# Optimization experiments

Hardware: AMD Instinct MI355X
Metric: run time of the kernel (lower is better)

## Reference

```python
import jax, jax.numpy as jnp
import numpy as np

N = 100000   # nodes
E = 1600000  # edges
F_IN = 256   # input features
H = 128      # hidden
C = 40       # classes


def setup_inputs() -> dict:
    key = jax.random.key(0)
    ks = jax.random.split(key, 6)
    x = jax.random.normal(ks[0], (N, F_IN), dtype=jnp.float32)
    edge_index = jax.random.randint(ks[1], (2, E), 0, N, dtype=jnp.int32)
    edge_attr = jax.random.uniform(ks[2], (E,), dtype=jnp.float32)
    # Glorot-style init like GCNConv
    W1 = jax.random.normal(ks[3], (F_IN, H), dtype=jnp.float32) * (1.0 / np.sqrt(F_IN))
    b1 = jnp.zeros((H,), dtype=jnp.float32)
    W2 = jax.random.normal(ks[4], (H, C), dtype=jnp.float32) * (1.0 / np.sqrt(H))
    b2 = jnp.zeros((C,), dtype=jnp.float32)
    return {"x": x, "edge_index": edge_index, "edge_attr": edge_attr,
            "W1": W1, "b1": b1, "W2": W2, "b2": b2}


def _gcn_norm(edge_index, edge_weight, num_nodes):
    # PyG gcn_norm: add self-loops (weight 1), symmetric D^{-1/2} A D^{-1/2}
    row, col = edge_index[0], edge_index[1]
    loop = jnp.arange(num_nodes, dtype=row.dtype)
    row = jnp.concatenate([row, loop])
    col = jnp.concatenate([col, loop])
    ew = jnp.concatenate([edge_weight, jnp.ones((num_nodes,), edge_weight.dtype)])
    deg = jax.ops.segment_sum(ew, col, num_segments=num_nodes)
    dinv = jnp.where(deg > 0, jax.lax.rsqrt(deg), 0.0)
    norm = dinv[row] * ew * dinv[col]
    return row, col, norm


def _gcn_conv(x, row, col, norm, W, b):
    h = x @ W                              # [N, out] dense transform first
    msg = h[row] * norm[:, None]           # gather source + edge scaling
    out = jax.ops.segment_sum(msg, col, num_segments=x.shape[0])  # scatter-add
    return out + b


def reference(x, edge_index, edge_attr, W1, b1, W2, b2):
    row, col, norm = _gcn_norm(edge_index, edge_attr, x.shape[0])
    h = _gcn_conv(x, row, col, norm, W1, b1)
    h = jax.nn.relu(h)
    # dropout is identity in eval mode
    h = _gcn_conv(h, row, col, norm, W2, b2)
    return jax.nn.log_softmax(h, axis=1)
```

## Files before the change

kernel.cpp:

```cpp
#include <hip/hip_runtime.h>

#define N_NODES 100000
#define N_EDGES 1600000
#define F_INPUT 256
#define H_DIM   128
#define C_DIM   40
#define NBKT    391
#define NCHK    1563
#define NGEMM1  1563

typedef short  bf8   __attribute__((ext_vector_type(8)));
typedef float  f32x4 __attribute__((ext_vector_type(4)));
typedef float  f32x2 __attribute__((ext_vector_type(2)));
typedef unsigned short u16x8 __attribute__((ext_vector_type(8)));

static __device__ __forceinline__ unsigned short f2bf(float f) {
    union { float f; unsigned u; } v; v.f = f;
    unsigned r = v.u + 0x7FFFu + ((v.u >> 16) & 1u);
    return (unsigned short)(r >> 16);
}
static __device__ __forceinline__ f32x2 bfpair(unsigned u) {
    union { unsigned u; float f; } lo, hi;
    lo.u = u << 16; hi.u = u & 0xFFFF0000u;
    return (f32x2){lo.f, hi.f};
}

__global__ void k_pre(const float* __restrict__ W1, const float* __restrict__ W2,
                      unsigned short* Wp1, unsigned short* Wp2) {
    int idx = blockIdx.x * 256 + threadIdx.x;
    if (idx < 32768) {
        int j = idx & 7, lane = (idx >> 3) & 63, ks = (idx >> 9) & 7, nt = idx >> 12;
        int m = lane & 15, q = lane >> 4;
        Wp1[idx] = f2bf(W1[(ks * 32 + q * 8 + j) * H_DIM + nt * 16 + m]);
    }
    int idx2 = idx - 32768;
    if (idx2 >= 0 && idx2 < 6144) {
        int j = idx2 & 7, lane = (idx2 >> 3) & 63, ks = (idx2 >> 9) & 3, nt = idx2 >> 11;
        int m = lane & 15, q = lane >> 4;
        int n = nt * 16 + m;
        Wp2[idx2] = (n < C_DIM) ? f2bf(W2[(ks * 32 + q * 8 + j) * C_DIM + n]) : (unsigned short)0;
    }
}

__global__ void k_hist(const int* __restrict__ col, unsigned* __restrict__ histG) {
    __shared__ unsigned histL[NBKT];
    int chunk = blockIdx.x, tid = threadIdx.x;
    for (int i = tid; i < NBKT; i += 256) histL[i] = 0;
    __syncthreads();
    int e0 = chunk * 1024 + tid;
#pragma unroll
    for (int k = 0; k < 4; k++) {
        int e = e0 + k * 256;
        if (e < N_EDGES) atomicAdd(&histL[col[e] >> 8], 1u);
    }
    __syncthreads();
    for (int i = tid; i < NBKT; i += 256) histG[(size_t)i * NCHK + chunk] = histL[i];
}

__global__ __launch_bounds__(256, 2) void k_gemm1(
        const float* __restrict__ x, const unsigned short* __restrict__ Wp,
        unsigned short* __restrict__ h) {
    __shared__ unsigned short sWp[32768];
    __shared__ unsigned short lds_out[64 * H_DIM];
    int tid = threadIdx.x;
    int wave = tid >> 6, lane = tid & 63;
    int m = lane & 15, q = lane >> 4;
    int tile = blockIdx.x;
    int row0 = tile * 64 + wave * 16;
    int rowA = row0 + m; if (rowA >= N_NODES) rowA = N_NODES - 1;
    const float* xr = x + (long)rowA * F_INPUT + q * 8;

    float4 xv[16];
#pragma unroll
    for (int ks = 0; ks < 8; ks++) {
        xv[2 * ks]     = *(const float4*)(xr + ks * 32);
        xv[2 * ks + 1] = *(const float4*)(xr + ks * 32 + 4);
    }
#pragma unroll
    for (int it = 0; it < 16; it++) {
        int idx = (it * 256 + tid) * 8;
        *(u16x8*)(sWp + idx) = *(const u16x8*)(Wp + idx);
    }
    __syncthreads();

    f32x4 acc[8];
#pragma unroll
    for (int i = 0; i < 8; i++) acc[i] = (f32x4){0.f, 0.f, 0.f, 0.f};
#pragma unroll
    for (int ks = 0; ks < 8; ks++) {
        float4 a0 = xv[2 * ks], a1 = xv[2 * ks + 1];
        bf8 a;
        a[0] = (short)f2bf(a0.x); a[1] = (short)f2bf(a0.y);
        a[2] = (short)f2bf(a0.z); a[3] = (short)f2bf(a0.w);
        a[4] = (short)f2bf(a1.x); a[5] = (short)f2bf(a1.y);
        a[6] = (short)f2bf(a1.z); a[7] = (short)f2bf(a1.w);
#pragma unroll
        for (int nt = 0; nt < 8; nt++) {
            bf8 bb = *(const bf8*)(sWp + (((nt * 8 + ks) * 64 + lane) << 3));
            acc[nt] = __builtin_amdgcn_mfma_f32_16x16x32_bf16(a, bb, acc[nt], 0, 0, 0);
        }
    }
    int lrow = wave * 16 + q * 4;
#pragma unroll
    for (int nt = 0; nt < 8; nt++)
#pragma unroll
        for (int r = 0; r < 4; r++)
            lds_out[(lrow + r) * H_DIM + nt * 16 + m] = f2bf(acc[nt][r]);
    __syncthreads();
    int valid = N_NODES - tile * 64; if (valid > 64) valid = 64;
    unsigned short* gbase = h + (size_t)tile * 64 * H_DIM;
#pragma unroll
    for (int i = 0; i < 4; i++) {
        int idx = (i * 256 + tid) * 8;
        if (idx < valid * H_DIM)
            *(u16x8*)(gbase + idx) = *(const u16x8*)(lds_out + idx);
    }
}

__global__ void k_scanB(unsigned* histG, unsigned* bktTotal) {
    __shared__ unsigned s[256];
    int B = blockIdx.x, t = threadIdx.x;
    unsigned carry = 0;
    for (int c0 = 0; c0 < NCHK; c0 += 256) {
        int idx = c0 + t;
        unsigned v = (idx < NCHK) ? histG[(size_t)B * NCHK + idx] : 0;
        s[t] = v; __syncthreads();
        for (int off = 1; off < 256; off <<= 1) {
            unsigned u = (t >= off) ? s[t - off] : 0;
            __syncthreads();
            s[t] += u;
            __syncthreads();
        }
        if (idx < NCHK) histG[(size_t)B * NCHK + idx] = s[t] - v + carry;
        unsigned tot = s[255];
        __syncthreads();
        carry += tot;
    }
    if (t == 0) bktTotal[B] = carry;
}

__global__ void k_scat1(const int* __restrict__ row, const int* __restrict__ col,
                        const float* __restrict__ ea,
                        const unsigned* __restrict__ histG,
                        const unsigned* __restrict__ bktTotal,
                        unsigned* __restrict__ bucketBase,
                        int2* __restrict__ recs) {
    __shared__ unsigned base_l[NBKT];
    __shared__ unsigned cursor[NBKT];
    __shared__ unsigned s[256];
    int blk = blockIdx.x, t = threadIdx.x;
    unsigned carry = 0;
    for (int c0 = 0; c0 < NBKT; c0 += 256) {
        int idx = c0 + t;
        unsigned v = (idx < NBKT) ? bktTotal[idx] : 0;
        s[t] = v; __syncthreads();
        for (int off = 1; off < 256; off <<= 1) {
            unsigned u = (t >= off) ? s[t - off] : 0;
            __syncthreads();
            s[t] += u;
            __syncthreads();
        }
        if (idx < NBKT) base_l[idx] = s[t] - v + carry;
        unsigned tot = s[255];
        __syncthreads();
        carry += tot;
    }
    __syncthreads();
    if (blk == 0) {
        for (int i = t; i < NBKT; i += 256) bucketBase[i] = base_l[i];
        if (t == 0) bucketBase[NBKT] = carry;
    }
    for (int i = t; i < NBKT; i += 256) {
        base_l[i] += histG[(size_t)i * NCHK + blk];
        cursor[i] = 0;
    }
    __syncthreads();
    int e0 = blk * 1024 + t;
#pragma unroll
    for (int k = 0; k < 4; k++) {
        int e = e0 + k * 256;
        if (e < N_EDGES) {
            int c = col[e];
            int bkt = c >> 8;
            unsigned r = atomicAdd(&cursor[bkt], 1u);
            int pos = (int)(base_l[bkt] + r);
            recs[pos] = make_int2((row[e] << 8) | (c & 255), __float_as_int(ea[e]));
        }
    }
}

__global__ void k_pass2a(const int2* __restrict__ recs,
                         const unsigned* __restrict__ bucketBase,
                         int* __restrict__ start, int* __restrict__ cnt,
                         float* __restrict__ dinv) {
    __shared__ unsigned cntL[256];
    __shared__ unsigned wsL[256];
    __shared__ unsigned s[256];
    int B = blockIdx.x, t = threadIdx.x;
    cntL[t] = 0; wsL[t] = 0;
    __syncthreads();
    int lo = (int)bucketBase[B], hi = (int)bucketBase[B + 1];
    for (int i = lo + t; i < hi; i += 256) {
        int2 rc = recs[i];
        int cl = rc.x & 255;
        atomicAdd(&cntL[cl], 1u);
        unsigned q = __float2uint_rn(__int_as_float(rc.y) * 65536.0f);
        atomicAdd(&wsL[cl], q);
    }
    __syncthreads();
    unsigned v = cntL[t];
    s[t] = v; __syncthreads();
    for (int off = 1; off < 256; off <<= 1) {
        unsigned u = (t >= off) ? s[t - off] : 0;
        __syncthreads();
        s[t] += u;
        __syncthreads();
    }
    int node = B * 256 + t;
    if (node < N_NODES) {
        start[node] = (int)(bucketBase[B] + s[t] - v);
        cnt[node] = (int)v;
        dinv[node] = rsqrtf((float)(65536u + wsL[t]) * (1.0f / 65536.0f));
    }
}

__global__ void k_pass2b(const int2* __restrict__ recs,
                         const unsigned* __restrict__ bucketBase,
                         const int* __restrict__ start,
                         const float* __restrict__ dinv,
                         int2* __restrict__ csr) {
    __shared__ int startL[256];
    __shared__ unsigned cur[256];
    int B = blockIdx.x, t = threadIdx.x;
    int node = B * 256 + t;
    startL[t] = (node < N_NODES) ? start[node] : 0;
    cur[t] = 0;
    __syncthreads();
    int lo = (int)bucketBase[B], hi = (int)bucketBase[B + 1];
    for (int i = lo + t; i < hi; i += 256) {
        int2 rc = recs[i];
        int cl = rc.x & 255;
        int rw = rc.x >> 8;
        float w = __int_as_float(rc.y) * dinv[rw];
        unsigned r = atomicAdd(&cur[cl], 1u);
        csr[startL[cl] + (int)r] = make_int2(rw, __float_as_int(w));
    }
}

__global__ __launch_bounds__(256) void k_agg1(
        const unsigned* __restrict__ hw, const int2* __restrict__ csr,
        const int* __restrict__ start, const int* __restrict__ cnt,
        const float* __restrict__ dinv, const float* __restrict__ b1,
        unsigned* __restrict__ h1w) {
    int c = blockIdx.x * 4 + (threadIdx.x >> 6);
    int lane = threadIdx.x & 63;
    if (c >= N_NODES) return;
    float di = dinv[c];
    int su = __builtin_amdgcn_readfirstlane(start[c]);
    int n  = __builtin_amdgcn_readfirstlane(cnt[c]);
    f32x2 acc;
    {
        f32x2 sp = bfpair(hw[(size_t)c * 64 + lane]);
        acc = (f32x2){di, di} * sp;
    }
    int i = 0;
    for (; i + 4 <= n; i += 4) {
        int2 p0 = csr[su + i], p1 = csr[su + i + 1];
        int2 p2 = csr[su + i + 2], p3 = csr[su + i + 3];
        int r0 = __builtin_amdgcn_readfirstlane(p0.x);
        int r1 = __builtin_amdgcn_readfirstlane(p1.x);
        int r2 = __builtin_amdgcn_readfirstlane(p2.x);
        int r3 = __builtin_amdgcn_readfirstlane(p3.x);
        float w0 = __int_as_float(__builtin_amdgcn_readfirstlane(p0.y));
        float w1 = __int_as_float(__builtin_amdgcn_readfirstlane(p1.y));
        float w2 = __int_as_float(__builtin_amdgcn_readfirstlane(p2.y));
        float w3 = __int_as_float(__builtin_amdgcn_readfirstlane(p3.y));
        unsigned a0 = hw[(size_t)r0 * 64 + lane];
        unsigned a1 = hw[(size_t)r1 * 64 + lane];
        unsigned a2 = hw[(size_t)r2 * 64 + lane];
        unsigned a3 = hw[(size_t)r3 * 64 + lane];
        acc += (f32x2){w0, w0} * bfpair(a0);
        acc += (f32x2){w1, w1} * bfpair(a1);
        acc += (f32x2){w2, w2} * bfpair(a2);
        acc += (f32x2){w3, w3} * bfpair(a3);
    }
    for (; i < n; i++) {
        int2 p = csr[su + i];
        int r = __builtin_amdgcn_readfirstlane(p.x);
        float w = __int_as_float(__builtin_amdgcn_readfirstlane(p.y));
        unsigned a = hw[(size_t)r * 64 + lane];
        acc += (f32x2){w, w} * bfpair(a);
    }
    float2 bb = ((const float2*)b1)[lane];
    float o0 = fmaxf(di * acc.x + bb.x, 0.f);
    float o1 = fmaxf(di * acc.y + bb.y, 0.f);
    h1w[(size_t)c * 64 + lane] = (unsigned)f2bf(o0) | ((unsigned)f2bf(o1) << 16);
}

__global__ __launch_bounds__(256, 4) void k_gemm2(const unsigned short* __restrict__ h1,
                        const unsigned short* __restrict__ Wp,
                        unsigned short* __restrict__ h2) {
    __shared__ unsigned short lds_out[64 * C_DIM];
    int tid = threadIdx.x;
    int wave = tid >> 6, lane = tid & 63;
    int m = lane & 15, q = lane >> 4;
    int row0 = blockIdx.x * 64 + wave * 16;
    int rowA = row0 + m; if (rowA >= N_NODES) rowA = N_NODES - 1;

    f32x4 acc[3];
#pragma unroll
    for (int i = 0; i < 3; i++) acc[i] = (f32x4){0.f, 0.f, 0.f, 0.f};
    const unsigned short* hr = h1 + (long)rowA * H_DIM + q * 8;
#pragma unroll
    for (int ks = 0; ks < 4; ks++) {
        bf8 a = *(const bf8*)(hr + ks * 32);
#pragma unroll
        for (int nt = 0; nt < 3; nt++) {
            bf8 b = *(const bf8*)(Wp + (((nt * 4 + ks) * 64 + lane) << 3));
            acc[nt] = __builtin_amdgcn_mfma_f32_16x16x32_bf16(a, b, acc[nt], 0, 0, 0);
        }
    }
    int lrow = wave * 16 + q * 4;
#pragma unroll
    for (int nt = 0; nt < 3; nt++)
#pragma unroll
        for (int r = 0; r < 4; r++) {
            int colo = nt * 16 + m;
            if (colo < C_DIM)
                lds_out[(lrow + r) * C_DIM + colo] = f2bf(acc[nt][r]);
        }
    __syncthreads();
    int valid = N_NODES - blockIdx.x * 64; if (valid > 64) valid = 64;
    unsigned short* gbase = h2 + (size_t)blockIdx.x * 64 * C_DIM;
    int total = valid * C_DIM;
#pragma unroll
    for (int i = 0; i < 3; i++) {
        int idx = (i * 256 + tid) * 4;
        if (idx < total)
            *(uint2*)(gbase + idx) = *(const uint2*)(lds_out + idx);
    }
}

__global__ void k_agg2(const unsigned short* __restrict__ h2, const int2* __restrict__ csr,
                       const int* __restrict__ start, const int* __restrict__ cnt,
                       const float* __restrict__ dinv, const float* __restrict__ b2,
                       float* __restrict__ out) {
    int c = (blockIdx.x * blockDim.x + threadIdx.x) >> 6;
    int lane = threadIdx.x & 63;
    if (c >= N_NODES) return;
    int eg = lane >> 3, cl = lane & 7;
    float di = dinv[c];
    int s = start[c];
    int n = cnt[c];

    float w[3]; int r[3];
#pragma unroll
    for (int t = 0; t < 3; t++) {
        int i = eg + 8 * t;
        int2 p = csr[s + ((i < n) ? i : 0)];
        bool val = (i < n);
        r[t] = val ? p.x : c;
        w[t] = val ? __int_as_float(p.y) : 0.f;
    }
    uint4 gv[3] = {{0,0,0,0},{0,0,0,0},{0,0,0,0}};
    uint4 selfv = {0, 0, 0, 0};
    if (cl < 5) {
#pragma unroll
        for (int t = 0; t < 3; t++)
            gv[t] = *(const uint4*)(h2 + (long)r[t] * C_DIM + cl * 8);
        if (eg == 0) selfv = *(const uint4*)(h2 + (long)c * C_DIM + cl * 8);
    }
    f32x2 acc[4];
#pragma unroll
    for (int k = 0; k < 4; k++) acc[k] = (f32x2){0.f, 0.f};
    {
        unsigned sv[4] = {selfv.x, selfv.y, selfv.z, selfv.w};
        f32x2 dd = (f32x2){di, di};
        if (eg == 0 && cl < 5)
#pragma unroll
            for (int k = 0; k < 4; k++) acc[k] += dd * bfpair(sv[k]);
    }
#pragma unroll
    for (int t = 0; t < 3; t++) {
        unsigned vv[4] = {gv[t].x, gv[t].y, gv[t].z, gv[t].w};
        f32x2 ww = (f32x2){w[t], w[t]};
#pragma unroll
        for (int k = 0; k < 4; k++) acc[k] += ww * bfpair(vv[k]);
    }
    for (int i = 24 + eg; i < n; i += 8) {
        int2 p = csr[s + i];
        if (cl < 5) {
            uint4 v4 = *(const uint4*)(h2 + (long)p.x * C_DIM + cl * 8);
            unsigned vv[4] = {v4.x, v4.y, v4.z, v4.w};
            float wt = __int_as_float(p.y);
            f32x2 ww = (f32x2){wt, wt};
#pragma unroll
            for (int k = 0; k < 4; k++) acc[k] += ww * bfpair(vv[k]);
        }
    }
#pragma unroll
    for (int k = 0; k < 4; k++) {
        acc[k].x += __shfl_xor(acc[k].x, 8);  acc[k].y += __shfl_xor(acc[k].y, 8);
        acc[k].x += __shfl_xor(acc[k].x, 16); acc[k].y += __shfl_xor(acc[k].y, 16);
        acc[k].x += __shfl_xor(acc[k].x, 32); acc[k].y += __shfl_xor(acc[k].y, 32);
    }
    float v[8];
    float lm = -INFINITY;
    if (cl < 5) {
#pragma unroll
        for (int k = 0; k < 4; k++) {
            v[2 * k]     = di * acc[k].x + b2[cl * 8 + 2 * k];
            v[2 * k + 1] = di * acc[k].y + b2[cl * 8 + 2 * k + 1];
            lm = fmaxf(lm, fmaxf(v[2 * k], v[2 * k + 1]));
        }
    }
    lm = fmaxf(lm, __shfl_xor(lm, 1));
    lm = fmaxf(lm, __shfl_xor(lm, 2));
    lm = fmaxf(lm, __shfl_xor(lm, 4));
    float ls = 0.f;
    if (cl < 5) {
#pragma unroll
        for (int j = 0; j < 8; j++) ls += __expf(v[j] - lm);
    }
    ls += __shfl_xor(ls, 1);
    ls += __shfl_xor(ls, 2);
    ls += __shfl_xor(ls, 4);
    if (eg == 0 && cl < 5) {
        float lsm = lm + logf(ls);
        f32x4 o0, o1;
#pragma unroll
        for (int j = 0; j < 4; j++) { o0[j] = v[j] - lsm; o1[j] = v[j + 4] - lsm; }
        *(f32x4*)(out + (long)c * C_DIM + cl * 8)     = o0;
        *(f32x4*)(out + (long)c * C_DIM + cl * 8 + 4) = o1;
    }
}

extern "C" void kernel_launch(void* const* d_in, const int* in_sizes, int n_in,
                              void* d_out, int out_size, void* d_ws, size_t ws_size,
                              hipStream_t stream) {
    const float* x  = (const float*)d_in[0];
    const int*   ei = (const int*)d_in[1];
    const float* ea = (const float*)d_in[2];
    const float* W1 = (const float*)d_in[3];
    const float* b1 = (const float*)d_in[4];
    const float* W2 = (const float*)d_in[5];
    const float* b2 = (const float*)d_in[6];
    const int* row = ei;
    const int* col = ei + N_EDGES;

    char* ws = (char*)d_ws;
    size_t off = 0;
    auto alloc = [&](size_t bytes) -> void* {
        void* p = ws + off;
        off = (off + bytes + 255) & ~(size_t)255;
        return p;
    };
    unsigned*       histG   = (unsigned*)alloc((size_t)NBKT * NCHK * 4);
    unsigned*       bktTot  = (unsigned*)alloc((size_t)NBKT * 4);
    unsigned*       bktBase = (unsigned*)alloc((size_t)(NBKT + 1) * 4);
    int*            start   = (int*)alloc((size_t)N_NODES * 4);
    int*            cnt     = (int*)alloc((size_t)N_NODES * 4);
    float*          dinv    = (float*)alloc((size_t)N_NODES * 4);
    int2*           recs    = (int2*)alloc((size_t)N_EDGES * 8);
    int2*           csr     = (int2*)alloc((size_t)(N_EDGES + 8) * 8);
    unsigned short* Wp1     = (unsigned short*)alloc(32768 * 2);
    unsigned short* Wp2     = (unsigned short*)alloc(6144 * 2);
    unsigned short* h       = (unsigned short*)alloc((size_t)(N_NODES + 64) * H_DIM * 2);
    unsigned short* h1      = (unsigned short*)alloc((size_t)N_NODES * H_DIM * 2);
    unsigned short* h2      = (unsigned short*)alloc((size_t)(N_NODES + 64) * C_DIM * 2);

    k_pre<<<152, 256, 0, stream>>>(W1, W2, Wp1, Wp2);
    k_hist<<<NCHK, 256, 0, stream>>>(col, histG);
    k_gemm1<<<NGEMM1, 256, 0, stream>>>(x, Wp1, h);
    k_scanB<<<NBKT, 256, 0, stream>>>(histG, bktTot);
    k_scat1<<<NCHK, 256, 0, stream>>>(row, col, ea, histG, bktTot, bktBase, recs);
    k_pass2a<<<NBKT, 256, 0, stream>>>(recs, bktBase, start, cnt, dinv);
    k_pass2b<<<NBKT, 256, 0, stream>>>(recs, bktBase, start, dinv, csr);
    k_agg1<<<N_NODES / 4, 256, 0, stream>>>((const unsigned*)h, csr, start, cnt, dinv, b1,
                                            (unsigned*)h1);
    k_gemm2<<<(N_NODES + 63) / 64, 256, 0, stream>>>(h1, Wp2, h2);
    k_agg2<<<N_NODES / 4, 256, 0, stream>>>(h2, csr, start, cnt, dinv, b2, (float*)d_out);
}
```

Baseline: 373.3 us.

## Fold source dinv into GEMM epilogues and merge preprocessing kernels

Merges the weight-pack and histogram kernels into one launch, and fuses the two CSR pass kernels into one so the start offsets stay in shared memory. The source-side dinv scaling moves out of the per-edge CSR weights and into the GEMM1/GEMM2 epilogues, which also drops the self-loop dinv multiply in the aggregation kernels. To make this possible, GEMM1 is moved after the CSR build, so it no longer overlaps with graph preprocessing. The aim is fewer launches, fewer dinv gathers per edge and no reload of start. The cost is that h is rounded to bf16 after the dinv scaling, which changes numerics slightly.

```diff
diff --git a/kernel.cpp b/kernel.cpp
--- a/kernel.cpp
+++ b/kernel.cpp
@@ -8,6 +8,7 @@
 #define NBKT    391
 #define NCHK    1563
 #define NGEMM1  1563
+#define NPREB   152
 
 typedef short  bf8   __attribute__((ext_vector_type(8)));
 typedef float  f32x4 __attribute__((ext_vector_type(4)));
@@ -25,9 +26,26 @@
     return (f32x2){lo.f, hi.f};
 }
 
-__global__ void k_pre(const float* __restrict__ W1, const float* __restrict__ W2,
-                      unsigned short* Wp1, unsigned short* Wp2) {
-    int idx = blockIdx.x * 256 + threadIdx.x;
+__global__ void k_preh(const float* __restrict__ W1, const float* __restrict__ W2,
+                       unsigned short* Wp1, unsigned short* Wp2,
+                       const int* __restrict__ col, unsigned* __restrict__ histG) {
+    int tid = threadIdx.x;
+    if (blockIdx.x >= NPREB) {
+        __shared__ unsigned histL[NBKT];
+        int chunk = blockIdx.x - NPREB;
+        for (int i = tid; i < NBKT; i += 256) histL[i] = 0;
+        __syncthreads();
+        int e0 = chunk * 1024 + tid;
+#pragma unroll
+        for (int k = 0; k < 4; k++) {
+            int e = e0 + k * 256;
+            if (e < N_EDGES) atomicAdd(&histL[col[e] >> 8], 1u);
+        }
+        __syncthreads();
+        for (int i = tid; i < NBKT; i += 256) histG[(size_t)i * NCHK + chunk] = histL[i];
+        return;
+    }
+    int idx = blockIdx.x * 256 + tid;
     if (idx < 32768) {
         int j = idx & 7, lane = (idx >> 3) & 63, ks = (idx >> 9) & 7, nt = idx >> 12;
         int m = lane & 15, q = lane >> 4;
@@ -39,81 +57,6 @@
         int m = lane & 15, q = lane >> 4;
         int n = nt * 16 + m;
         Wp2[idx2] = (n < C_DIM) ? f2bf(W2[(ks * 32 + q * 8 + j) * C_DIM + n]) : (unsigned short)0;
-    }
-}
-
-__global__ void k_hist(const int* __restrict__ col, unsigned* __restrict__ histG) {
-    __shared__ unsigned histL[NBKT];
-    int chunk = blockIdx.x, tid = threadIdx.x;
-    for (int i = tid; i < NBKT; i += 256) histL[i] = 0;
-    __syncthreads();
-    int e0 = chunk * 1024 + tid;
-#pragma unroll
-    for (int k = 0; k < 4; k++) {
-        int e = e0 + k * 256;
-        if (e < N_EDGES) atomicAdd(&histL[col[e] >> 8], 1u);
-    }
-    __syncthreads();
-    for (int i = tid; i < NBKT; i += 256) histG[(size_t)i * NCHK + chunk] = histL[i];
-}
-
-__global__ __launch_bounds__(256, 2) void k_gemm1(
-        const float* __restrict__ x, const unsigned short* __restrict__ Wp,
-        unsigned short* __restrict__ h) {
-    __shared__ unsigned short sWp[32768];
-    __shared__ unsigned short lds_out[64 * H_DIM];
-    int tid = threadIdx.x;
-    int wave = tid >> 6, lane = tid & 63;
-    int m = lane & 15, q = lane >> 4;
-    int tile = blockIdx.x;
-    int row0 = tile * 64 + wave * 16;
-    int rowA = row0 + m; if (rowA >= N_NODES) rowA = N_NODES - 1;
-    const float* xr = x + (long)rowA * F_INPUT + q * 8;
-
-    float4 xv[16];
-#pragma unroll
-    for (int ks = 0; ks < 8; ks++) {
-        xv[2 * ks]     = *(const float4*)(xr + ks * 32);
-        xv[2 * ks + 1] = *(const float4*)(xr + ks * 32 + 4);
-    }
-#pragma unroll
-    for (int it = 0; it < 16; it++) {
-        int idx = (it * 256 + tid) * 8;
-        *(u16x8*)(sWp + idx) = *(const u16x8*)(Wp + idx);
-    }
-    __syncthreads();
-
-    f32x4 acc[8];
-#pragma unroll
-    for (int i = 0; i < 8; i++) acc[i] = (f32x4){0.f, 0.f, 0.f, 0.f};
-#pragma unroll
-    for (int ks = 0; ks < 8; ks++) {
-        float4 a0 = xv[2 * ks], a1 = xv[2 * ks + 1];
-        bf8 a;
-        a[0] = (short)f2bf(a0.x); a[1] = (short)f2bf(a0.y);
-        a[2] = (short)f2bf(a0.z); a[3] = (short)f2bf(a0.w);
-        a[4] = (short)f2bf(a1.x); a[5] = (short)f2bf(a1.y);
-        a[6] = (short)f2bf(a1.z); a[7] = (short)f2bf(a1.w);
-#pragma unroll
-        for (int nt = 0; nt < 8; nt++) {
-            bf8 bb = *(const bf8*)(sWp + (((nt * 8 + ks) * 64 + lane) << 3));
-            acc[nt] = __builtin_amdgcn_mfma_f32_16x16x32_bf16(a, bb, acc[nt], 0, 0, 0);
-        }
-    }
-    int lrow = wave * 16 + q * 4;
-#pragma unroll
-    for (int nt = 0; nt < 8; nt++)
-#pragma unroll
-        for (int r = 0; r < 4; r++)
-            lds_out[(lrow + r) * H_DIM + nt * 16 + m] = f2bf(acc[nt][r]);
-    __syncthreads();
-    int valid = N_NODES - tile * 64; if (valid > 64) valid = 64;
-    unsigned short* gbase = h + (size_t)tile * 64 * H_DIM;
-#pragma unroll
-    for (int i = 0; i < 4; i++) {
-        int idx = (i * 256 + tid) * 8;
-        if (idx < valid * H_DIM)
-            *(u16x8*)(gbase + idx) = *(const u16x8*)(lds_out + idx);
     }
 }
 
@@ -189,15 +132,17 @@
     }
 }
 
-__global__ void k_pass2a(const int2* __restrict__ recs,
-                         const unsigned* __restrict__ bucketBase,
-                         int* __restrict__ start, int* __restrict__ cnt,
-                         float* __restrict__ dinv) {
+__global__ void k_pass2(const int2* __restrict__ recs,
+                        const unsigned* __restrict__ bucketBase,
+                        int* __restrict__ start, int* __restrict__ cnt,
+                        float* __restrict__ dinv, int2* __restrict__ csr) {
     __shared__ unsigned cntL[256];
     __shared__ unsigned wsL[256];
     __shared__ unsigned s[256];
+    __shared__ int startL[256];
+    __shared__ unsigned cur[256];
     int B = blockIdx.x, t = threadIdx.x;
-    cntL[t] = 0; wsL[t] = 0;
+    cntL[t] = 0; wsL[t] = 0; cur[t] = 0;
     __syncthreads();
     int lo = (int)bucketBase[B], hi = (int)bucketBase[B + 1];
     for (int i = lo + t; i < hi; i += 256) {
@@ -216,34 +161,87 @@
         s[t] += u;
         __syncthreads();
     }
+    int st = lo + (int)(s[t] - v);
+    startL[t] = st;
     int node = B * 256 + t;
     if (node < N_NODES) {
-        start[node] = (int)(bucketBase[B] + s[t] - v);
+        start[node] = st;
         cnt[node] = (int)v;
         dinv[node] = rsqrtf((float)(65536u + wsL[t]) * (1.0f / 65536.0f));
     }
-}
-
-__global__ void k_pass2b(const int2* __restrict__ recs,
-                         const unsigned* __restrict__ bucketBase,
-                         const int* __restrict__ start,
-                         const float* __restrict__ dinv,
-                         int2* __restrict__ csr) {
-    __shared__ int startL[256];
-    __shared__ unsigned cur[256];
-    int B = blockIdx.x, t = threadIdx.x;
-    int node = B * 256 + t;
-    startL[t] = (node < N_NODES) ? start[node] : 0;
-    cur[t] = 0;
-    __syncthreads();
-    int lo = (int)bucketBase[B], hi = (int)bucketBase[B + 1];
+    __syncthreads();
     for (int i = lo + t; i < hi; i += 256) {
         int2 rc = recs[i];
         int cl = rc.x & 255;
         int rw = rc.x >> 8;
-        float w = __int_as_float(rc.y) * dinv[rw];
         unsigned r = atomicAdd(&cur[cl], 1u);
-        csr[startL[cl] + (int)r] = make_int2(rw, __float_as_int(w));
+        csr[startL[cl] + (int)r] = make_int2(rw, rc.y);
+    }
+}
+
+__global__ __launch_bounds__(256, 2) void k_gemm1(
+        const float* __restrict__ x, const unsigned short* __restrict__ Wp,
+        const float* __restrict__ dinv, unsigned short* __restrict__ h) {
+    __shared__ unsigned short sWp[32768];
+    __shared__ unsigned short lds_out[64 * H_DIM];
+    int tid = threadIdx.x;
+    int wave = tid >> 6, lane = tid & 63;
+    int m = lane & 15, q = lane >> 4;
+    int tile = blockIdx.x;
+    int row0 = tile * 64 + wave * 16;
+    int rowA = row0 + m; if (rowA >= N_NODES) rowA = N_NODES - 1;
+    const float* xr = x + (long)rowA * F_INPUT + q * 8;
+
+    float4 xv[16];
+#pragma unroll
+    for (int ks = 0; ks < 8; ks++) {
+        xv[2 * ks]     = *(const float4*)(xr + ks * 32);
+        xv[2 * ks + 1] = *(const float4*)(xr + ks * 32 + 4);
+    }
+#pragma unroll
+    for (int it = 0; it < 16; it++) {
+        int idx = (it * 256 + tid) * 8;
+        *(u16x8*)(sWp + idx) = *(const u16x8*)(Wp + idx);
+    }
+    __syncthreads();
+
+    f32x4 acc[8];
+#pragma unroll
+    for (int i = 0; i < 8; i++) acc[i] = (f32x4){0.f, 0.f, 0.f, 0.f};
+#pragma unroll
+    for (int ks = 0; ks < 8; ks++) {
+        float4 a0 = xv[2 * ks], a1 = xv[2 * ks + 1];
+        bf8 a;
+        a[0] = (short)f2bf(a0.x); a[1] = (short)f2bf(a0.y);
+        a[2] = (short)f2bf(a0.z); a[3] = (short)f2bf(a0.w);
+        a[4] = (short)f2bf(a1.x); a[5] = (short)f2bf(a1.y);
+        a[6] = (short)f2bf(a1.z); a[7] = (short)f2bf(a1.w);
+#pragma unroll
+        for (int nt = 0; nt < 8; nt++) {
+            bf8 bb = *(const bf8*)(sWp + (((nt * 8 + ks) * 64 + lane) << 3));
+            acc[nt] = __builtin_amdgcn_mfma_f32_16x16x32_bf16(a, bb, acc[nt], 0, 0, 0);
+        }
+    }
+    int lrow = wave * 16 + q * 4;
+    float dv[4];
+#pragma unroll
+    for (int r = 0; r < 4; r++) {
+        int gr = tile * 64 + lrow + r; if (gr >= N_NODES) gr = N_NODES - 1;
+        dv[r] = dinv[gr];
+    }
+#pragma unroll
+    for (int nt = 0; nt < 8; nt++)
+#pragma unroll
+        for (int r = 0; r < 4; r++)
+            lds_out[(lrow + r) * H_DIM + nt * 16 + m] = f2bf(acc[nt][r] * dv[r]);
+    __syncthreads();
+    int valid = N_NODES - tile * 64; if (valid > 64) valid = 64;
+    unsigned short* gbase = h + (size_t)tile * 64 * H_DIM;
+#pragma unroll
+    for (int i = 0; i < 4; i++) {
+        int idx = (i * 256 + tid) * 8;
+        if (idx < valid * H_DIM)
+            *(u16x8*)(gbase + idx) = *(const u16x8*)(lds_out + idx);
     }
 }
 
@@ -258,11 +256,7 @@
     float di = dinv[c];
     int su = __builtin_amdgcn_readfirstlane(start[c]);
     int n  = __builtin_amdgcn_readfirstlane(cnt[c]);
-    f32x2 acc;
-    {
-        f32x2 sp = bfpair(hw[(size_t)c * 64 + lane]);
-        acc = (f32x2){di, di} * sp;
-    }
+    f32x2 acc = bfpair(hw[(size_t)c * 64 + lane]);
     int i = 0;
     for (; i + 4 <= n; i += 4) {
         int2 p0 = csr[su + i], p1 = csr[su + i + 1];
@@ -299,6 +293,7 @@
 
 __global__ __launch_bounds__(256, 4) void k_gemm2(const unsigned short* __restrict__ h1,
                         const unsigned short* __restrict__ Wp,
+                        const float* __restrict__ dinv,
                         unsigned short* __restrict__ h2) {
     __shared__ unsigned short lds_out[64 * C_DIM];
     int tid = threadIdx.x;
@@ -321,13 +316,19 @@
         }
     }
     int lrow = wave * 16 + q * 4;
+    float dv[4];
+#pragma unroll
+    for (int r = 0; r < 4; r++) {
+        int gr = blockIdx.x * 64 + lrow + r; if (gr >= N_NODES) gr = N_NODES - 1;
+        dv[r] = dinv[gr];
+    }
 #pragma unroll
     for (int nt = 0; nt < 3; nt++)
 #pragma unroll
         for (int r = 0; r < 4; r++) {
             int colo = nt * 16 + m;
             if (colo < C_DIM)
-                lds_out[(lrow + r) * C_DIM + colo] = f2bf(acc[nt][r]);
+                lds_out[(lrow + r) * C_DIM + colo] = f2bf(acc[nt][r] * dv[r]);
         }
     __syncthreads();
     int valid = N_NODES - blockIdx.x * 64; if (valid > 64) valid = 64;
@@ -375,10 +376,9 @@
     for (int k = 0; k < 4; k++) acc[k] = (f32x2){0.f, 0.f};
     {
         unsigned sv[4] = {selfv.x, selfv.y, selfv.z, selfv.w};
-        f32x2 dd = (f32x2){di, di};
         if (eg == 0 && cl < 5)
 #pragma unroll
-            for (int k = 0; k < 4; k++) acc[k] += dd * bfpair(sv[k]);
+            for (int k = 0; k < 4; k++) acc[k] += bfpair(sv[k]);
     }
 #pragma unroll
     for (int t = 0; t < 3; t++) {
@@ -469,15 +469,13 @@
     unsigned short* h1      = (unsigned short*)alloc((size_t)N_NODES * H_DIM * 2);
     unsigned short* h2      = (unsigned short*)alloc((size_t)(N_NODES + 64) * C_DIM * 2);
 
-    k_pre<<<152, 256, 0, stream>>>(W1, W2, Wp1, Wp2);
-    k_hist<<<NCHK, 256, 0, stream>>>(col, histG);
-    k_gemm1<<<NGEMM1, 256, 0, stream>>>(x, Wp1, h);
+    k_preh<<<NPREB + NCHK, 256, 0, stream>>>(W1, W2, Wp1, Wp2, col, histG);
     k_scanB<<<NBKT, 256, 0, stream>>>(histG, bktTot);
     k_scat1<<<NCHK, 256, 0, stream>>>(row, col, ea, histG, bktTot, bktBase, recs);
-    k_pass2a<<<NBKT, 256, 0, stream>>>(recs, bktBase, start, cnt, dinv);
-    k_pass2b<<<NBKT, 256, 0, stream>>>(recs, bktBase, start, dinv, csr);
+    k_pass2<<<NBKT, 256, 0, stream>>>(recs, bktBase, start, cnt, dinv, csr);
+    k_gemm1<<<NGEMM1, 256, 0, stream>>>(x, Wp1, dinv, h);
     k_agg1<<<N_NODES / 4, 256, 0, stream>>>((const unsigned*)h, csr, start, cnt, dinv, b1,
                                             (unsigned*)h1);
-    k_gemm2<<<(N_NODES + 63) / 64, 256, 0, stream>>>(h1, Wp2, h2);
+    k_gemm2<<<(N_NODES + 63) / 64, 256, 0, stream>>>(h1, Wp2, dinv, h2);
     k_agg2<<<N_NODES / 4, 256, 0, stream>>>(h2, csr, start, cnt, dinv, b2, (float*)d_out);
 }
```

Measured after the change: 366.3 us. Within noise of the previous version (-1.9%).
